# Kernel optimization log

Hardware: AMD Instinct MI355X
Metric: run time of the kernel (lower is better)

Reference implementation:

```python
import jax, jax.numpy as jnp
import numpy as np

N_NODES = 50000
N_EDGES = 800000
D_IN = 96
D_OUT = 96
NEG_SLOPE = 0.2


def setup_inputs() -> dict:
    key = jax.random.key(0)
    k1, k2, k3, k4, k5 = jax.random.split(key, 5)
    x = jax.random.normal(k1, (N_NODES, D_IN), dtype=jnp.float32)
    W = jax.random.normal(k2, (D_IN, D_OUT), dtype=jnp.float32) * (1.0 / np.sqrt(D_IN))
    att_src = jax.random.normal(k3, (D_OUT,), dtype=jnp.float32) * 0.1
    att_dst = jax.random.normal(k4, (D_OUT,), dtype=jnp.float32) * 0.1
    bias = jnp.zeros((D_OUT,), dtype=jnp.float32)
    edge_index = jax.random.randint(k5, (2, N_EDGES), 0, N_NODES, dtype=jnp.int64)
    return {"x": x, "W": W, "att_src": att_src, "att_dst": att_dst,
            "bias": bias, "edge_index": edge_index}


def reference(x, W, att_src, att_dst, bias, edge_index):
    N = x.shape[0]
    # Linear transform: h = x W   [N, D_out]
    h = x @ W
    # PyG GATConv default add_self_loops=True
    loops = jnp.arange(N, dtype=edge_index.dtype)
    src = jnp.concatenate([edge_index[0], loops])  # message source j
    dst = jnp.concatenate([edge_index[1], loops])  # aggregation target i
    # Per-node attention halves, gathered per edge
    a_src = h @ att_src  # [N]
    a_dst = h @ att_dst  # [N]
    e = jax.nn.leaky_relu(a_src[src] + a_dst[dst], NEG_SLOPE)  # [E+N]
    # Segment softmax over edges sharing the same destination
    m = jax.ops.segment_max(e, dst, num_segments=N)  # every node has a self-loop
    e = jnp.exp(e - m[dst])
    denom = jax.ops.segment_sum(e, dst, num_segments=N)
    alpha = e / (denom[dst] + 1e-16)  # [E+N]
    # Weighted scatter-aggregate of source features
    out = jax.ops.segment_sum(h[src] * alpha[:, None], dst, num_segments=N)
    return jnp.tanh(out + bias)
```

## Files before the change

### kernel.cpp

```cpp
#include <hip/hip_runtime.h>
#include <hip/hip_bf16.h>
#include <cstdint>

#define N_NODES 50000
#define N_EDGES 800000
#define D 96
#define NEG_SLOPE 0.2f
#define R1ROWS 16
#define BUCKET 64
#define NXCD 8
#define DST_PER_PART (N_NODES / NXCD)

__global__ __launch_bounds__(384) void k1_gemm(
    const float* __restrict__ x, const float* __restrict__ W,
    float* __restrict__ hf, __hip_bfloat16* __restrict__ hb) {
    __shared__ float Ws[D][D];
    __shared__ float xs[R1ROWS][D];
    const int tx = threadIdx.x, ty = threadIdx.y;
    const int t = ty * 96 + tx;
    const size_t row0 = (size_t)blockIdx.x * R1ROWS;

    {
        const float4* W4 = (const float4*)W;
        float4* Ws4 = (float4*)Ws;
#pragma unroll
        for (int i = 0; i < 6; ++i) Ws4[t + 384 * i] = W4[t + 384 * i];
        const float4* x4 = (const float4*)(x + row0 * D);
        ((float4*)xs)[t] = x4[t];
    }
    __syncthreads();

    float acc0 = 0.f, acc1 = 0.f, acc2 = 0.f, acc3 = 0.f;
#pragma unroll
    for (int k = 0; k < D; k += 4) {
        float4 xa = *(const float4*)&xs[ty][k];
        float4 xb = *(const float4*)&xs[ty + 4][k];
        float4 xc = *(const float4*)&xs[ty + 8][k];
        float4 xd = *(const float4*)&xs[ty + 12][k];
        float w0 = Ws[k][tx], w1 = Ws[k + 1][tx], w2 = Ws[k + 2][tx], w3 = Ws[k + 3][tx];
        acc0 += xa.x * w0 + xa.y * w1 + xa.z * w2 + xa.w * w3;
        acc1 += xb.x * w0 + xb.y * w1 + xb.z * w2 + xb.w * w3;
        acc2 += xc.x * w0 + xc.y * w1 + xc.z * w2 + xc.w * w3;
        acc3 += xd.x * w0 + xd.y * w1 + xd.z * w2 + xd.w * w3;
    }
    hf[(row0 + ty     ) * D + tx] = acc0;
    hf[(row0 + ty + 4 ) * D + tx] = acc1;
    hf[(row0 + ty + 8 ) * D + tx] = acc2;
    hf[(row0 + ty + 12) * D + tx] = acc3;
    hb[(row0 + ty     ) * D + tx] = __float2bfloat16(acc0);
    hb[(row0 + ty + 4 ) * D + tx] = __float2bfloat16(acc1);
    hb[(row0 + ty + 8 ) * D + tx] = __float2bfloat16(acc2);
    hb[(row0 + ty + 12) * D + tx] = __float2bfloat16(acc3);
}

__global__ __launch_bounds__(256) void k1b_att(
    const float* __restrict__ hf, const float* __restrict__ att_src,
    const float* __restrict__ att_dst, float* __restrict__ a_src,
    float* __restrict__ a_dst) {
    const int lane = threadIdx.x & 63;
    const int row = (blockIdx.x * 256 + threadIdx.x) >> 6;
    if (row >= N_NODES) return;
    float s = 0.f, d = 0.f;
    if (lane < 48) {
        float2 hv = *(const float2*)(hf + (size_t)row * D + lane * 2);
        float2 as = *(const float2*)(att_src + lane * 2);
        float2 ad = *(const float2*)(att_dst + lane * 2);
        s = hv.x * as.x + hv.y * as.y;
        d = hv.x * ad.x + hv.y * ad.y;
    }
#pragma unroll
    for (int off = 32; off >= 1; off >>= 1) {
        s += __shfl_down(s, off);
        d += __shfl_down(d, off);
    }
    if (lane == 0) { a_src[row] = s; a_dst[row] = d; }
}

__global__ void k_bucket(const int* __restrict__ ei,
                         const float* __restrict__ a_src, const float* __restrict__ a_dst,
                         int* __restrict__ cnt, uint* __restrict__ bkt) {
    const int part = blockIdx.x & (NXCD - 1);
    const int e = (blockIdx.x >> 3) * 256 + threadIdx.x;
    if (e >= N_EDGES) return;
    int d = ei[N_EDGES + e];
    if (d / DST_PER_PART != part) return;
    int s = ei[e];
    float v = a_src[s] + a_dst[d];
    v = v > 0.f ? v : NEG_SLOPE * v;
    float w = __expf(v);
    uint u = __float_as_uint(w);
    uint wb = (u + 0x7FFFu + ((u >> 16) & 1u)) & 0xFFFF0000u;
    uint pk = wb | (uint)s;
    int pos = atomicAdd(&cnt[d], 1);
    if (pos < BUCKET) bkt[(size_t)d * BUCKET + pos] = pk;
}

__global__ __launch_bounds__(256) void k_gather(
    const int* __restrict__ cnt, const uint* __restrict__ bkt,
    const float* __restrict__ a_src, const float* __restrict__ a_dst,
    const __hip_bfloat16* __restrict__ hb, const float* __restrict__ bias,
    float* __restrict__ out) {
    const int lane = threadIdx.x & 63;
    const int node = (blockIdx.x * 256 + threadIdx.x) >> 6;
    if (node >= N_NODES) return;
    const uint* __restrict__ hbu = (const uint*)hb;
    const uint* __restrict__ bucket = bkt + (size_t)node * BUCKET;
    const int cn = min(cnt[node], BUCKET);

    float es = a_src[node] + a_dst[node];
    es = es > 0.f ? es : NEG_SLOPE * es;
    float wself = __expf(es);
    uint pself = hbu[(size_t)node * 48 + lane];
    float acc0 = __uint_as_float(pself << 16) * wself;
    float acc1 = __uint_as_float(pself & 0xffff0000u) * wself;
    float wsum = wself;

    int k = 0;
    for (; k + 3 < cn; k += 4) {
        uint e0 = bucket[k], e1 = bucket[k + 1], e2 = bucket[k + 2], e3 = bucket[k + 3];
        uint p0 = hbu[(size_t)(e0 & 0xFFFFu) * 48 + lane];
        uint p1 = hbu[(size_t)(e1 & 0xFFFFu) * 48 + lane];
        uint p2 = hbu[(size_t)(e2 & 0xFFFFu) * 48 + lane];
        uint p3 = hbu[(size_t)(e3 & 0xFFFFu) * 48 + lane];
        float w0 = __uint_as_float(e0 & 0xFFFF0000u);
        float w1 = __uint_as_float(e1 & 0xFFFF0000u);
        float w2 = __uint_as_float(e2 & 0xFFFF0000u);
        float w3 = __uint_as_float(e3 & 0xFFFF0000u);
        acc0 += __uint_as_float(p0 << 16) * w0 + __uint_as_float(p1 << 16) * w1
              + __uint_as_float(p2 << 16) * w2 + __uint_as_float(p3 << 16) * w3;
        acc1 += __uint_as_float(p0 & 0xffff0000u) * w0 + __uint_as_float(p1 & 0xffff0000u) * w1
              + __uint_as_float(p2 & 0xffff0000u) * w2 + __uint_as_float(p3 & 0xffff0000u) * w3;
        wsum += w0 + w1 + w2 + w3;
    }
    for (; k < cn; ++k) {
        uint e0 = bucket[k];
        uint p0 = hbu[(size_t)(e0 & 0xFFFFu) * 48 + lane];
        float w0 = __uint_as_float(e0 & 0xFFFF0000u);
        acc0 += __uint_as_float(p0 << 16) * w0;
        acc1 += __uint_as_float(p0 & 0xffff0000u) * w0;
        wsum += w0;
    }

    if (lane < 48) {
        float inv = 1.f / (wsum + 1e-16f);
        float2 bv = *(const float2*)(bias + lane * 2);
        float2 o;
        o.x = tanhf(acc0 * inv + bv.x);
        o.y = tanhf(acc1 * inv + bv.y);
        *(float2*)(out + (size_t)node * D + lane * 2) = o;
    }
}

extern "C" void kernel_launch(void* const* d_in, const int* in_sizes, int n_in,
                              void* d_out, int out_size, void* d_ws, size_t ws_size,
                              hipStream_t stream) {
    const float* x       = (const float*)d_in[0];
    const float* W       = (const float*)d_in[1];
    const float* att_src = (const float*)d_in[2];
    const float* att_dst = (const float*)d_in[3];
    const float* bias    = (const float*)d_in[4];
    const int*   ei      = (const int*)d_in[5];
    float* out = (float*)d_out;

    float* hf = out;

    char* ws = (char*)d_ws;
    __hip_bfloat16* hb = (__hip_bfloat16*)ws; ws += (size_t)N_NODES * D * 2;
    float* a_src  = (float*)ws; ws += (size_t)N_NODES * 4;
    float* a_dst  = (float*)ws; ws += (size_t)N_NODES * 4;
    int*   cnt    = (int*)ws;   ws += (size_t)N_NODES * 4;
    uint*  bkt    = (uint*)ws;  ws += (size_t)N_NODES * BUCKET * 4;

    hipMemsetAsync(cnt, 0, (size_t)N_NODES * 4, stream);
    k1_gemm<<<N_NODES / R1ROWS, dim3(96, 4), 0, stream>>>(x, W, hf, hb);
    k1b_att<<<(N_NODES * 64 + 255) / 256, 256, 0, stream>>>(hf, att_src, att_dst, a_src, a_dst);
    k_bucket<<<((N_EDGES + 255) / 256) * NXCD, 256, 0, stream>>>(ei, a_src, a_dst, cnt, bkt);
    k_gather<<<(N_NODES * 64 + 255) / 256, 256, 0, stream>>>(cnt, bkt, a_src, a_dst, hb, bias, out);
}
```

Measured before the change: 124.5 us.

## Precompute W·att projections, drop fp32 h store, fold memset, widen gather unroll

The attention scores are now computed straight from x using precomputed vectors W·att_src and W·att_dst, produced by a tiny one-block kernel. The GEMM therefore no longer writes an fp32 copy of h, and the attention kernel reads x instead of h. The counter memset moves into the attention kernel, and the GEMM launch is reordered after bucketing. The gather loop is unrolled to 16 with vectorized bucket loads and 32-bit index math to raise memory-level parallelism; summation order changes slightly.

```diff
diff --git a/kernel.cpp b/kernel.cpp
--- a/kernel.cpp
+++ b/kernel.cpp
@@ -11,9 +11,37 @@
 #define NXCD 8
 #define DST_PER_PART (N_NODES / NXCD)
 
+__global__ __launch_bounds__(384) void k0_proj(
+    const float* __restrict__ W, const float* __restrict__ att_src,
+    const float* __restrict__ att_dst, float* __restrict__ p_src,
+    float* __restrict__ p_dst) {
+    __shared__ float Wl[D * (D + 1)];
+    __shared__ float asl[D], adl[D];
+    __shared__ float rs[4][D], rd[4][D];
+    const int tx = threadIdx.x, ty = threadIdx.y;
+    const int t = ty * 96 + tx;
+    for (int i = t; i < D * D; i += 384) Wl[(i / D) * (D + 1) + (i % D)] = W[i];
+    if (t < D) { asl[t] = att_src[t]; adl[t] = att_dst[t]; }
+    __syncthreads();
+    float ps = 0.f, pd = 0.f;
+    const float* wrow = &Wl[tx * (D + 1) + ty * 24];
+#pragma unroll
+    for (int c = 0; c < 24; ++c) {
+        float w = wrow[c];
+        ps += w * asl[ty * 24 + c];
+        pd += w * adl[ty * 24 + c];
+    }
+    rs[ty][tx] = ps; rd[ty][tx] = pd;
+    __syncthreads();
+    if (ty == 0) {
+        p_src[tx] = rs[0][tx] + rs[1][tx] + rs[2][tx] + rs[3][tx];
+        p_dst[tx] = rd[0][tx] + rd[1][tx] + rd[2][tx] + rd[3][tx];
+    }
+}
+
 __global__ __launch_bounds__(384) void k1_gemm(
     const float* __restrict__ x, const float* __restrict__ W,
-    float* __restrict__ hf, __hip_bfloat16* __restrict__ hb) {
+    __hip_bfloat16* __restrict__ hb) {
     __shared__ float Ws[D][D];
     __shared__ float xs[R1ROWS][D];
     const int tx = threadIdx.x, ty = threadIdx.y;
@@ -43,10 +71,6 @@
         acc2 += xc.x * w0 + xc.y * w1 + xc.z * w2 + xc.w * w3;
         acc3 += xd.x * w0 + xd.y * w1 + xd.z * w2 + xd.w * w3;
     }
-    hf[(row0 + ty     ) * D + tx] = acc0;
-    hf[(row0 + ty + 4 ) * D + tx] = acc1;
-    hf[(row0 + ty + 8 ) * D + tx] = acc2;
-    hf[(row0 + ty + 12) * D + tx] = acc3;
     hb[(row0 + ty     ) * D + tx] = __float2bfloat16(acc0);
     hb[(row0 + ty + 4 ) * D + tx] = __float2bfloat16(acc1);
     hb[(row0 + ty + 8 ) * D + tx] = __float2bfloat16(acc2);
@@ -54,26 +78,26 @@
 }
 
 __global__ __launch_bounds__(256) void k1b_att(
-    const float* __restrict__ hf, const float* __restrict__ att_src,
-    const float* __restrict__ att_dst, float* __restrict__ a_src,
-    float* __restrict__ a_dst) {
+    const float* __restrict__ x, const float* __restrict__ p_src,
+    const float* __restrict__ p_dst, float* __restrict__ a_src,
+    float* __restrict__ a_dst, int* __restrict__ cnt) {
     const int lane = threadIdx.x & 63;
     const int row = (blockIdx.x * 256 + threadIdx.x) >> 6;
     if (row >= N_NODES) return;
     float s = 0.f, d = 0.f;
     if (lane < 48) {
-        float2 hv = *(const float2*)(hf + (size_t)row * D + lane * 2);
-        float2 as = *(const float2*)(att_src + lane * 2);
-        float2 ad = *(const float2*)(att_dst + lane * 2);
-        s = hv.x * as.x + hv.y * as.y;
-        d = hv.x * ad.x + hv.y * ad.y;
+        float2 xv = *(const float2*)(x + (size_t)row * D + lane * 2);
+        float2 ps = *(const float2*)(p_src + lane * 2);
+        float2 pd = *(const float2*)(p_dst + lane * 2);
+        s = xv.x * ps.x + xv.y * ps.y;
+        d = xv.x * pd.x + xv.y * pd.y;
     }
 #pragma unroll
     for (int off = 32; off >= 1; off >>= 1) {
         s += __shfl_down(s, off);
         d += __shfl_down(d, off);
     }
-    if (lane == 0) { a_src[row] = s; a_dst[row] = d; }
+    if (lane == 0) { a_src[row] = s; a_dst[row] = d; cnt[row] = 0; }
 }
 
 __global__ void k_bucket(const int* __restrict__ ei,
@@ -83,7 +107,8 @@
     const int e = (blockIdx.x >> 3) * 256 + threadIdx.x;
     if (e >= N_EDGES) return;
     int d = ei[N_EDGES + e];
-    if (d / DST_PER_PART != part) return;
+    int lo = part * DST_PER_PART;
+    if (d < lo || d >= lo + DST_PER_PART) return;
     int s = ei[e];
     float v = a_src[s] + a_dst[d];
     v = v > 0.f ? v : NEG_SLOPE * v;
@@ -100,7 +125,7 @@
     const float* __restrict__ a_src, const float* __restrict__ a_dst,
     const __hip_bfloat16* __restrict__ hb, const float* __restrict__ bias,
     float* __restrict__ out) {
-    const int lane = threadIdx.x & 63;
+    const uint lane = threadIdx.x & 63;
     const int node = (blockIdx.x * 256 + threadIdx.x) >> 6;
     if (node >= N_NODES) return;
     const uint* __restrict__ hbu = (const uint*)hb;
@@ -110,31 +135,63 @@
     float es = a_src[node] + a_dst[node];
     es = es > 0.f ? es : NEG_SLOPE * es;
     float wself = __expf(es);
-    uint pself = hbu[(size_t)node * 48 + lane];
+    uint pself = hbu[(uint)node * 48u + lane];
     float acc0 = __uint_as_float(pself << 16) * wself;
     float acc1 = __uint_as_float(pself & 0xffff0000u) * wself;
     float wsum = wself;
 
     int k = 0;
-    for (; k + 3 < cn; k += 4) {
-        uint e0 = bucket[k], e1 = bucket[k + 1], e2 = bucket[k + 2], e3 = bucket[k + 3];
-        uint p0 = hbu[(size_t)(e0 & 0xFFFFu) * 48 + lane];
-        uint p1 = hbu[(size_t)(e1 & 0xFFFFu) * 48 + lane];
-        uint p2 = hbu[(size_t)(e2 & 0xFFFFu) * 48 + lane];
-        uint p3 = hbu[(size_t)(e3 & 0xFFFFu) * 48 + lane];
-        float w0 = __uint_as_float(e0 & 0xFFFF0000u);
-        float w1 = __uint_as_float(e1 & 0xFFFF0000u);
-        float w2 = __uint_as_float(e2 & 0xFFFF0000u);
-        float w3 = __uint_as_float(e3 & 0xFFFF0000u);
-        acc0 += __uint_as_float(p0 << 16) * w0 + __uint_as_float(p1 << 16) * w1
-              + __uint_as_float(p2 << 16) * w2 + __uint_as_float(p3 << 16) * w3;
-        acc1 += __uint_as_float(p0 & 0xffff0000u) * w0 + __uint_as_float(p1 & 0xffff0000u) * w1
-              + __uint_as_float(p2 & 0xffff0000u) * w2 + __uint_as_float(p3 & 0xffff0000u) * w3;
-        wsum += w0 + w1 + w2 + w3;
+    for (; k + 15 < cn; k += 16) {
+        uint b[16];
+        *(uint4*)&b[0]  = *(const uint4*)&bucket[k];
+        *(uint4*)&b[4]  = *(const uint4*)&bucket[k + 4];
+        *(uint4*)&b[8]  = *(const uint4*)&bucket[k + 8];
+        *(uint4*)&b[12] = *(const uint4*)&bucket[k + 12];
+        uint p[16];
+#pragma unroll
+        for (int j = 0; j < 16; ++j) p[j] = hbu[(b[j] & 0xFFFFu) * 48u + lane];
+#pragma unroll
+        for (int j = 0; j < 16; ++j) {
+            float w = __uint_as_float(b[j] & 0xFFFF0000u);
+            acc0 += __uint_as_float(p[j] << 16) * w;
+            acc1 += __uint_as_float(p[j] & 0xffff0000u) * w;
+            wsum += w;
+        }
+    }
+    if (k + 7 < cn) {
+        uint b[8];
+        *(uint4*)&b[0] = *(const uint4*)&bucket[k];
+        *(uint4*)&b[4] = *(const uint4*)&bucket[k + 4];
+        uint p[8];
+#pragma unroll
+        for (int j = 0; j < 8; ++j) p[j] = hbu[(b[j] & 0xFFFFu) * 48u + lane];
+#pragma unroll
+        for (int j = 0; j < 8; ++j) {
+            float w = __uint_as_float(b[j] & 0xFFFF0000u);
+            acc0 += __uint_as_float(p[j] << 16) * w;
+            acc1 += __uint_as_float(p[j] & 0xffff0000u) * w;
+            wsum += w;
+        }
+        k += 8;
+    }
+    if (k + 3 < cn) {
+        uint b[4];
+        *(uint4*)&b[0] = *(const uint4*)&bucket[k];
+        uint p[4];
+#pragma unroll
+        for (int j = 0; j < 4; ++j) p[j] = hbu[(b[j] & 0xFFFFu) * 48u + lane];
+#pragma unroll
+        for (int j = 0; j < 4; ++j) {
+            float w = __uint_as_float(b[j] & 0xFFFF0000u);
+            acc0 += __uint_as_float(p[j] << 16) * w;
+            acc1 += __uint_as_float(p[j] & 0xffff0000u) * w;
+            wsum += w;
+        }
+        k += 4;
     }
     for (; k < cn; ++k) {
         uint e0 = bucket[k];
-        uint p0 = hbu[(size_t)(e0 & 0xFFFFu) * 48 + lane];
+        uint p0 = hbu[(e0 & 0xFFFFu) * 48u + lane];
         float w0 = __uint_as_float(e0 & 0xFFFF0000u);
         acc0 += __uint_as_float(p0 << 16) * w0;
         acc1 += __uint_as_float(p0 & 0xffff0000u) * w0;
@@ -162,18 +219,18 @@
     const int*   ei      = (const int*)d_in[5];
     float* out = (float*)d_out;
 
-    float* hf = out;
-
     char* ws = (char*)d_ws;
     __hip_bfloat16* hb = (__hip_bfloat16*)ws; ws += (size_t)N_NODES * D * 2;
     float* a_src  = (float*)ws; ws += (size_t)N_NODES * 4;
     float* a_dst  = (float*)ws; ws += (size_t)N_NODES * 4;
     int*   cnt    = (int*)ws;   ws += (size_t)N_NODES * 4;
+    float* p_src  = (float*)ws; ws += (size_t)D * 4;
+    float* p_dst  = (float*)ws; ws += (size_t)D * 4;
     uint*  bkt    = (uint*)ws;  ws += (size_t)N_NODES * BUCKET * 4;
 
-    hipMemsetAsync(cnt, 0, (size_t)N_NODES * 4, stream);
-    k1_gemm<<<N_NODES / R1ROWS, dim3(96, 4), 0, stream>>>(x, W, hf, hb);
-    k1b_att<<<(N_NODES * 64 + 255) / 256, 256, 0, stream>>>(hf, att_src, att_dst, a_src, a_dst);
+    k0_proj<<<1, dim3(96, 4), 0, stream>>>(W, att_src, att_dst, p_src, p_dst);
+    k1b_att<<<(N_NODES * 64 + 255) / 256, 256, 0, stream>>>(x, p_src, p_dst, a_src, a_dst, cnt);
     k_bucket<<<((N_EDGES + 255) / 256) * NXCD, 256, 0, stream>>>(ei, a_src, a_dst, cnt, bkt);
+    k1_gemm<<<N_NODES / R1ROWS, dim3(96, 4), 0, stream>>>(x, W, hb);
     k_gather<<<(N_NODES * 64 + 255) / 256, 256, 0, stream>>>(cnt, bkt, a_src, a_dst, hb, bias, out);
 }
```

New measurement: 120.6 us. 3.2% less time.
